# Kernel optimization log

Measured on AMD Instinct MI355X. Metric: run time of the kernel, lower is better.

The kernel has to match this reference:

```python
import jax, jax.numpy as jnp
import numpy as np

D_MODEL = 2048
NUM_EXPERTS = 64
TOP_K = 4
N_TOKENS = 16384


def setup_inputs() -> dict:
    key = jax.random.key(0)
    k_u, k_e = jax.random.split(key)
    u = jax.random.normal(k_u, (N_TOKENS, D_MODEL), dtype=jnp.float32)
    # E initialized like torch.randn(d_model, num_experts) * 0.01
    E = jax.random.normal(k_e, (D_MODEL, NUM_EXPERTS), dtype=jnp.float32) * 0.01
    bias = jnp.zeros((NUM_EXPERTS,), dtype=jnp.float32)
    return {"u": u, "E": E, "bias": bias}


def reference(u, E, bias):
    # logits: [N, num_experts]
    logits = u @ E + bias
    scores = jax.nn.softmax(logits, axis=-1)
    # torch.topk returns values sorted descending; lax.top_k matches
    topk_s, topk_i = jax.lax.top_k(scores, TOP_K)
    aux_loss = jnp.sum(jnp.mean(scores, axis=0) ** 2) * NUM_EXPERTS
    return (topk_i, topk_s, scores, aux_loss)
```

## Files before the change

### kernel.cpp

```cpp
#include <hip/hip_runtime.h>
#include <math.h>

#define N_TOK 16384
#define DM    2048
#define NE    64
#define TOPK  4

#define OFF_TI  0
#define OFF_TS  (N_TOK * TOPK)
#define OFF_SC  (2 * N_TOK * TOPK)
#define OFF_AUX (2 * N_TOK * TOPK + N_TOK * NE)

#define MTPB  16
#define RW    256
#define NRND  (DM / RW)
#define RSTR  264
#define PLN   (MTPB * RSTR)

#define EH_OFF   1024
#define ET_ELEMS ((size_t)NE * DM)
#define WS_NEED  (EH_OFF + 4 * ET_ELEMS)

typedef short s8v __attribute__((ext_vector_type(8)));
typedef float f4v __attribute__((ext_vector_type(4)));

__device__ __forceinline__ unsigned short bf16_rne(float x) {
  unsigned int b = __float_as_uint(x);
  b += 0x7FFFu + ((b >> 16) & 1u);
  return (unsigned short)(b >> 16);
}

__global__ __launch_bounds__(256) void router_prep(
    const float* __restrict__ E, unsigned short* __restrict__ eh,
    unsigned short* __restrict__ el)
{
  __shared__ float t[32][65];
  const int tid = threadIdx.x;
  const int k0  = blockIdx.x * 32;
#pragma unroll
  for (int i = 0; i < 2; ++i) {
    const int fi = i * 256 + tid;
    const int kk = fi >> 4, ee = (fi & 15) * 4;
    const float4 v = *(const float4*)(E + (size_t)(k0 + kk) * NE + ee);
    t[kk][ee] = v.x; t[kk][ee + 1] = v.y; t[kk][ee + 2] = v.z; t[kk][ee + 3] = v.w;
  }
  __syncthreads();
  const int j    = tid >> 6;
  const int lane = tid & 63;
  const int ex   = j * 16 + (lane & 15);
  const int kb   = (lane >> 4) * 8;
  unsigned int hw[4], lw[4];
#pragma unroll
  for (int p = 0; p < 4; ++p) {
    unsigned short h[2], l[2];
#pragma unroll
    for (int q = 0; q < 2; ++q) {
      const float x = t[kb + p * 2 + q][ex];
      h[q] = bf16_rne(x);
      l[q] = bf16_rne(x - __uint_as_float((unsigned)h[q] << 16));
    }
    hw[p] = (unsigned)h[0] | ((unsigned)h[1] << 16);
    lw[p] = (unsigned)l[0] | ((unsigned)l[1] << 16);
  }
  const size_t o = (size_t)blockIdx.x * 2048 + j * 512 + lane * 8;
  *(uint4*)(eh + o) = make_uint4(hw[0], hw[1], hw[2], hw[3]);
  *(uint4*)(el + o) = make_uint4(lw[0], lw[1], lw[2], lw[3]);
}

#define LOAD_U(pf, r) do { _Pragma("unroll") \
  for (int i_ = 0; i_ < 4; ++i_) \
    pf[i_] = *(const float4*)(ugp + (size_t)(r) * RW + i_ * 64); } while (0)

#define WRITE_U(pf, base) do { _Pragma("unroll") \
  for (int i_ = 0; i_ < 4; ++i_) { \
    const float4 v_ = pf[i_]; \
    const unsigned short h0_ = bf16_rne(v_.x), h1_ = bf16_rne(v_.y), \
                         h2_ = bf16_rne(v_.z), h3_ = bf16_rne(v_.w); \
    const unsigned short l0_ = bf16_rne(v_.x - __uint_as_float((unsigned)h0_ << 16)); \
    const unsigned short l1_ = bf16_rne(v_.y - __uint_as_float((unsigned)h1_ << 16)); \
    const unsigned short l2_ = bf16_rne(v_.z - __uint_as_float((unsigned)h2_ << 16)); \
    const unsigned short l3_ = bf16_rne(v_.w - __uint_as_float((unsigned)h3_ << 16)); \
    *(uint2*)&sh[(base) + uoff + i_ * 64] = \
      make_uint2((unsigned)h0_ | ((unsigned)h1_ << 16), (unsigned)h2_ | ((unsigned)h3_ << 16)); \
    *(uint2*)&sh[(base) + PLN + uoff + i_ * 64] = \
      make_uint2((unsigned)l0_ | ((unsigned)l1_ << 16), (unsigned)l2_ | ((unsigned)l3_ << 16)); \
  } } while (0)

#define COMPUTE(r, base) do { _Pragma("unroll") \
  for (int ks_ = 0; ks_ < 2; ++ks_) { \
    const s8v ah_ = *(const s8v*)&sh[(base) + a_off + ks_ * 32]; \
    const s8v al_ = *(const s8v*)&sh[(base) + PLN + a_off + ks_ * 32]; \
    const size_t pb_ = (size_t)(((r) * 8 + kq * 2 + ks_) * 2048) + lane * 8; \
    _Pragma("unroll") for (int j_ = 0; j_ < 4; ++j_) { \
      const s8v bh_ = *(const s8v*)&eh[pb_ + j_ * 512]; \
      const s8v bl_ = *(const s8v*)&el[pb_ + j_ * 512]; \
      acc[j_] = __builtin_amdgcn_mfma_f32_16x16x32_bf16(ah_, bh_, acc[j_], 0, 0, 0); \
      acc[j_] = __builtin_amdgcn_mfma_f32_16x16x32_bf16(ah_, bl_, acc[j_], 0, 0, 0); \
      acc[j_] = __builtin_amdgcn_mfma_f32_16x16x32_bf16(al_, bh_, acc[j_], 0, 0, 0); \
      acc[j_] = __builtin_amdgcn_mfma_f32_16x16x32_bf16(al_, bl_, acc[j_], 0, 0, 0); \
    } } } while (0)

__global__ __launch_bounds__(256, 4) void router_main_mfma(
    const float* __restrict__ u, const unsigned short* __restrict__ eh,
    const unsigned short* __restrict__ el, const float* __restrict__ bias,
    float* __restrict__ out, float* __restrict__ ws)
{
  __shared__ __align__(16) unsigned short sh[4 * PLN];

  const int tid  = threadIdx.x;
  const int lane = tid & 63;
  const int kq   = __builtin_amdgcn_readfirstlane(tid >> 6);
  const int lm   = lane & 15;
  const int lk   = lane >> 4;
  const int tok0 = blockIdx.x * MTPB;

  const int srow = tid >> 4, sseg = tid & 15;
  const float* ugp = u + (size_t)(tok0 + srow) * DM + sseg * 4;
  const int uoff = srow * RSTR + sseg * 4;

  const int a_off = lm * RSTR + kq * 64 + lk * 8;

  f4v acc[4];
#pragma unroll
  for (int j = 0; j < 4; ++j) acc[j] = (f4v){0.f, 0.f, 0.f, 0.f};

  float4 pfA[4], pfB[4];
  LOAD_U(pfA, 0);
  LOAD_U(pfB, 1);
  WRITE_U(pfA, 0);
  __syncthreads();

  for (int rr = 0; rr < NRND; rr += 2) {
    WRITE_U(pfB, 2 * PLN);
    if (rr + 2 < NRND) LOAD_U(pfA, rr + 2);
    COMPUTE(rr, 0);
    __syncthreads();
    if (rr + 2 < NRND) WRITE_U(pfA, 0);
    if (rr + 3 < NRND) LOAD_U(pfB, rr + 3);
    COMPUTE(rr + 1, 2 * PLN);
    __syncthreads();
  }

  float* fin = (float*)sh;
#pragma unroll
  for (int j = 0; j < 4; ++j)
#pragma unroll
    for (int q = 0; q < 4; ++q)
      fin[kq * (16 * 68) + (lk * 4 + q) * 68 + j * 16 + lm] = acc[j][q];
  __syncthreads();

  const float be = bias[lane];
  float asum = 0.f;
#pragma unroll
  for (int tt = 0; tt < 4; ++tt) {
    const int t = kq * 4 + tt;
    float x = fin[t * 68 + lane] + fin[1 * 1088 + t * 68 + lane]
            + fin[2 * 1088 + t * 68 + lane] + fin[3 * 1088 + t * 68 + lane] + be;

    float m = x;
#pragma unroll
    for (int off = 32; off > 0; off >>= 1) m = fmaxf(m, __shfl_xor(m, off));
    float p = expf(x - m);
    float s = p;
#pragma unroll
    for (int off = 32; off > 0; off >>= 1) s += __shfl_xor(s, off);
    float sc = p / s;

    out[OFF_SC + (size_t)(tok0 + t) * NE + lane] = sc;
    asum += sc;

    float v = sc;
#pragma unroll
    for (int k = 0; k < TOPK; ++k) {
      float bv = v;
      int   bi = lane;
#pragma unroll
      for (int off = 32; off > 0; off >>= 1) {
        float ov = __shfl_xor(bv, off);
        int   oi = __shfl_xor(bi, off);
        if (ov > bv || (ov == bv && oi < bi)) { bv = ov; bi = oi; }
      }
      if (lane == k) {
        out[OFF_TI + (size_t)(tok0 + t) * TOPK + k] = (float)bi;
        out[OFF_TS + (size_t)(tok0 + t) * TOPK + k] = bv;
      }
      if (lane == bi) v = -INFINITY;
    }
  }
  atomicAdd(&ws[lane], asum);
}

#define TPB     64
#define FB_DC   32
#define FB_NCH  (1024 / FB_DC)
#define FB_LSTR 68
#define FB_UB   (TPB * FB_LSTR)
#define FB_EOFF (2 * FB_UB)
#define FB_EB   (2 * FB_DC * NE)

__global__ __launch_bounds__(1024, 4) void router_main_fb(
    const float* __restrict__ u, const float* __restrict__ E,
    const float* __restrict__ bias, float* __restrict__ out,
    float* __restrict__ ws)
{
  __shared__ float smem[FB_EOFF + 2 * FB_EB];

  const int tid  = threadIdx.x;
  const int lane = tid & 63;
  const int wid  = __builtin_amdgcn_readfirstlane(tid >> 6);
  const int eg   = wid & 7;
  const int kh   = wid >> 3;
  const int tok0 = blockIdx.x * TPB;

  const int stok  = tid >> 4;
  const int sdseg = tid & 15;
  const int skh   = sdseg >> 3;
  const int sdsub = (sdseg & 7) * 4;
  const float* sgbase = u + (size_t)(tok0 + stok) * DM + skh * 1024 + sdsub;
  float* swp = smem + stok * FB_LSTR + sdseg * 4;

  const int eq  = tid & 511;
  const int ekh = tid >> 9;
  const float* egbase = E + (size_t)ekh * 1024 * NE + eq * 4;
  float* ewp = smem + FB_EOFF + ekh * (FB_DC * NE) + eq * 4;

  float acc[8];
#pragma unroll
  for (int j = 0; j < 8; ++j) acc[j] = 0.f;

  float4 pf[3];
  pf[0] = *(const float4*)(sgbase + 0 * FB_DC);
  pf[1] = *(const float4*)(sgbase + 1 * FB_DC);
  pf[2] = *(const float4*)(sgbase + 2 * FB_DC);
  float4 epf = *(const float4*)(egbase + 0 * (FB_DC * NE));
  *(float4*)(swp + 0) = pf[0];
  *(float4*)(ewp + 0) = epf;
  epf = *(const float4*)(egbase + 1 * (FB_DC * NE));
  __syncthreads();

  for (int c = 0; c < FB_NCH; ++c) {
    if (c + 1 < FB_NCH) {
      *(float4*)(swp + ((c + 1) & 1) * FB_UB) = pf[(c + 1) % 3];
      *(float4*)(ewp + ((c + 1) & 1) * FB_EB) = epf;
    }
    if (c + 2 < FB_NCH)
      epf = *(const float4*)(egbase + (c + 2) * (FB_DC * NE));
    if (c + 3 < FB_NCH)
      pf[c % 3] = *(const float4*)(sgbase + (c + 3) * FB_DC);

    const float* sb = smem + (c & 1) * FB_UB + lane * FB_LSTR + kh * FB_DC;
    const float* eb = smem + FB_EOFF + (c & 1) * FB_EB + kh * (FB_DC * NE) + eg * 8;
#pragma unroll
    for (int s = 0; s < 8; ++s) {
      float4 uf = *(const float4*)(sb + s * 4);
#pragma unroll
      for (int dd = 0; dd < 4; ++dd) {
        const float* er = eb + (s * 4 + dd) * NE;
        float4 e0 = *(const float4*)(er);
        float4 e1 = *(const float4*)(er + 4);
        const float uv = (&uf.x)[dd];
        acc[0] = fmaf(e0.x, uv, acc[0]);
        acc[1] = fmaf(e0.y, uv, acc[1]);
        acc[2] = fmaf(e0.z, uv, acc[2]);
        acc[3] = fmaf(e0.w, uv, acc[3]);
        acc[4] = fmaf(e1.x, uv, acc[4]);
        acc[5] = fmaf(e1.y, uv, acc[5]);
        acc[6] = fmaf(e1.z, uv, acc[6]);
        acc[7] = fmaf(e1.w, uv, acc[7]);
      }
    }
    __syncthreads();
  }

  float* fin = smem;
  if (kh == 0) {
#pragma unroll
    for (int j = 0; j < 8; ++j) fin[lane * 65 + eg * 8 + j] = acc[j];
  }
  __syncthreads();
  if (kh == 1) {
#pragma unroll
    for (int j = 0; j < 8; ++j) fin[lane * 65 + eg * 8 + j] += acc[j];
  }
  __syncthreads();

  const float be = bias[lane];
  float asum = 0.f;
#pragma unroll
  for (int tt = 0; tt < 4; ++tt) {
    const int t = wid * 4 + tt;
    float x = fin[t * 65 + lane] + be;

    float m = x;
#pragma unroll
    for (int off = 32; off > 0; off >>= 1) m = fmaxf(m, __shfl_xor(m, off));
    float p = expf(x - m);
    float s = p;
#pragma unroll
    for (int off = 32; off > 0; off >>= 1) s += __shfl_xor(s, off);
    float sc = p / s;

    out[OFF_SC + (size_t)(tok0 + t) * NE + lane] = sc;
    asum += sc;

    float v = sc;
#pragma unroll
    for (int k = 0; k < TOPK; ++k) {
      float bv = v;
      int   bi = lane;
#pragma unroll
      for (int off = 32; off > 0; off >>= 1) {
        float ov = __shfl_xor(bv, off);
        int   oi = __shfl_xor(bi, off);
        if (ov > bv || (ov == bv && oi < bi)) { bv = ov; bi = oi; }
      }
      if (lane == k) {
        out[OFF_TI + (size_t)(tok0 + t) * TOPK + k] = (float)bi;
        out[OFF_TS + (size_t)(tok0 + t) * TOPK + k] = bv;
      }
      if (lane == bi) v = -INFINITY;
    }
  }
  atomicAdd(&ws[lane], asum);
}

__global__ void router_aux(const float* __restrict__ ws, float* __restrict__ out)
{
  const int lane = threadIdx.x & 63;
  float m = ws[lane] * (1.0f / N_TOK);
  float v = m * m;
#pragma unroll
  for (int off = 32; off > 0; off >>= 1) v += __shfl_xor(v, off);
  if (lane == 0) out[OFF_AUX] = v * (float)NE;
}

extern "C" void kernel_launch(void* const* d_in, const int* in_sizes, int n_in,
                              void* d_out, int out_size, void* d_ws, size_t ws_size,
                              hipStream_t stream) {
  const float* u    = (const float*)d_in[0];
  const float* E    = (const float*)d_in[1];
  const float* bias = (const float*)d_in[2];
  float* out = (float*)d_out;
  float* ws  = (float*)d_ws;

  hipMemsetAsync(ws, 0, NE * sizeof(float), stream);
  if (ws_size >= WS_NEED) {
    unsigned short* eh = (unsigned short*)((char*)ws + EH_OFF);
    unsigned short* el = eh + ET_ELEMS;
    router_prep<<<DM / 32, 256, 0, stream>>>(E, eh, el);
    router_main_mfma<<<N_TOK / MTPB, 256, 0, stream>>>(u, eh, el, bias, out, ws);
  } else {
    router_main_fb<<<N_TOK / TPB, 1024, 0, stream>>>(u, E, bias, out, ws);
  }
  router_aux<<<1, 64, 0, stream>>>(ws, out);
}
```

Before: 313.7 us.

## Enlarge token tile to 64 per block and fuse aux reduction into main kernel

The MFMA router kernel now handles 64 tokens per block instead of 16, using a narrower 128-wide K round. Each wave's E fragments (hi/lo bf16) are reused across four 16-token sub-tiles, so global/L2 traffic for E per token drops fourfold. Cross-wave partial sums are reduced in two passes through shared memory. The workspace memset and the separate aux kernel are replaced by zeroing inside the prep kernel and a last-block-done atomic counter that computes aux_loss. The trade-offs are more accumulator registers (occupancy hint lowered to 1), only 256 blocks in the grid, and a serial 16-token epilogue per wave.

New measurement: 273.6 us. 1.15x faster.

```diff
diff --git a/kernel.cpp b/kernel.cpp
--- a/kernel.cpp
+++ b/kernel.cpp
@@ -11,11 +11,11 @@
 #define OFF_SC  (2 * N_TOK * TOPK)
 #define OFF_AUX (2 * N_TOK * TOPK + N_TOK * NE)
 
-#define MTPB  16
-#define RW    256
+#define MTPB  64
+#define RW    128
 #define NRND  (DM / RW)
-#define RSTR  264
-#define PLN   (MTPB * RSTR)
+#define KSTR  136
+#define PLN   (MTPB * KSTR)
 
 #define EH_OFF   1024
 #define ET_ELEMS ((size_t)NE * DM)
@@ -32,10 +32,11 @@
 
 __global__ __launch_bounds__(256) void router_prep(
     const float* __restrict__ E, unsigned short* __restrict__ eh,
-    unsigned short* __restrict__ el)
+    unsigned short* __restrict__ el, float* __restrict__ ws)
 {
   __shared__ float t[32][65];
   const int tid = threadIdx.x;
+  if (blockIdx.x == 0 && tid < 128) ws[tid] = 0.f;
   const int k0  = blockIdx.x * 32;
 #pragma unroll
   for (int i = 0; i < 2; ++i) {
@@ -68,11 +69,11 @@
 }
 
 #define LOAD_U(pf, r) do { _Pragma("unroll") \
-  for (int i_ = 0; i_ < 4; ++i_) \
-    pf[i_] = *(const float4*)(ugp + (size_t)(r) * RW + i_ * 64); } while (0)
+  for (int i_ = 0; i_ < 8; ++i_) \
+    pf[i_] = *(const float4*)(ugp + (size_t)(r) * RW + i_ * 16); } while (0)
 
 #define WRITE_U(pf, base) do { _Pragma("unroll") \
-  for (int i_ = 0; i_ < 4; ++i_) { \
+  for (int i_ = 0; i_ < 8; ++i_) { \
     const float4 v_ = pf[i_]; \
     const unsigned short h0_ = bf16_rne(v_.x), h1_ = bf16_rne(v_.y), \
                          h2_ = bf16_rne(v_.z), h3_ = bf16_rne(v_.w); \
@@ -80,27 +81,31 @@
     const unsigned short l1_ = bf16_rne(v_.y - __uint_as_float((unsigned)h1_ << 16)); \
     const unsigned short l2_ = bf16_rne(v_.z - __uint_as_float((unsigned)h2_ << 16)); \
     const unsigned short l3_ = bf16_rne(v_.w - __uint_as_float((unsigned)h3_ << 16)); \
-    *(uint2*)&sh[(base) + uoff + i_ * 64] = \
+    *(uint2*)&sh[(base) + uoff + i_ * 16] = \
       make_uint2((unsigned)h0_ | ((unsigned)h1_ << 16), (unsigned)h2_ | ((unsigned)h3_ << 16)); \
-    *(uint2*)&sh[(base) + PLN + uoff + i_ * 64] = \
+    *(uint2*)&sh[(base) + PLN + uoff + i_ * 16] = \
       make_uint2((unsigned)l0_ | ((unsigned)l1_ << 16), (unsigned)l2_ | ((unsigned)l3_ << 16)); \
   } } while (0)
 
-#define COMPUTE(r, base) do { _Pragma("unroll") \
-  for (int ks_ = 0; ks_ < 2; ++ks_) { \
-    const s8v ah_ = *(const s8v*)&sh[(base) + a_off + ks_ * 32]; \
-    const s8v al_ = *(const s8v*)&sh[(base) + PLN + a_off + ks_ * 32]; \
-    const size_t pb_ = (size_t)(((r) * 8 + kq * 2 + ks_) * 2048) + lane * 8; \
+#define COMPUTE(r, base) do { \
+    const int    pk_ = (r) * 4 + kq; \
+    const size_t pb_ = (size_t)pk_ * 2048 + lane * 8; \
+    s8v ah_[4], al_[4]; \
+    _Pragma("unroll") for (int tt_ = 0; tt_ < 4; ++tt_) { \
+      ah_[tt_] = *(const s8v*)&sh[(base) + a_off + tt_ * (16 * KSTR)]; \
+      al_[tt_] = *(const s8v*)&sh[(base) + PLN + a_off + tt_ * (16 * KSTR)]; \
+    } \
     _Pragma("unroll") for (int j_ = 0; j_ < 4; ++j_) { \
       const s8v bh_ = *(const s8v*)&eh[pb_ + j_ * 512]; \
       const s8v bl_ = *(const s8v*)&el[pb_ + j_ * 512]; \
-      acc[j_] = __builtin_amdgcn_mfma_f32_16x16x32_bf16(ah_, bh_, acc[j_], 0, 0, 0); \
-      acc[j_] = __builtin_amdgcn_mfma_f32_16x16x32_bf16(ah_, bl_, acc[j_], 0, 0, 0); \
-      acc[j_] = __builtin_amdgcn_mfma_f32_16x16x32_bf16(al_, bh_, acc[j_], 0, 0, 0); \
-      acc[j_] = __builtin_amdgcn_mfma_f32_16x16x32_bf16(al_, bl_, acc[j_], 0, 0, 0); \
-    } } } while (0)
-
-__global__ __launch_bounds__(256, 4) void router_main_mfma(
+      _Pragma("unroll") for (int tt_ = 0; tt_ < 4; ++tt_) { \
+        acc[tt_][j_] = __builtin_amdgcn_mfma_f32_16x16x32_bf16(ah_[tt_], bh_, acc[tt_][j_], 0, 0, 0); \
+        acc[tt_][j_] = __builtin_amdgcn_mfma_f32_16x16x32_bf16(ah_[tt_], bl_, acc[tt_][j_], 0, 0, 0); \
+        acc[tt_][j_] = __builtin_amdgcn_mfma_f32_16x16x32_bf16(al_[tt_], bh_, acc[tt_][j_], 0, 0, 0); \
+        acc[tt_][j_] = __builtin_amdgcn_mfma_f32_16x16x32_bf16(al_[tt_], bl_, acc[tt_][j_], 0, 0, 0); \
+      } } } while (0)
+
+__global__ __launch_bounds__(256, 1) void router_main_mfma(
     const float* __restrict__ u, const unsigned short* __restrict__ eh,
     const unsigned short* __restrict__ el, const float* __restrict__ bias,
     float* __restrict__ out, float* __restrict__ ws)
@@ -114,17 +119,19 @@
   const int lk   = lane >> 4;
   const int tok0 = blockIdx.x * MTPB;
 
-  const int srow = tid >> 4, sseg = tid & 15;
+  const int srow = tid >> 2, sseg = tid & 3;
   const float* ugp = u + (size_t)(tok0 + srow) * DM + sseg * 4;
-  const int uoff = srow * RSTR + sseg * 4;
-
-  const int a_off = lm * RSTR + kq * 64 + lk * 8;
-
-  f4v acc[4];
-#pragma unroll
-  for (int j = 0; j < 4; ++j) acc[j] = (f4v){0.f, 0.f, 0.f, 0.f};
-
-  float4 pfA[4], pfB[4];
+  const int uoff = srow * KSTR + sseg * 4;
+
+  const int a_off = lm * KSTR + kq * 32 + lk * 8;
+
+  f4v acc[4][4];
+#pragma unroll
+  for (int t = 0; t < 4; ++t)
+#pragma unroll
+    for (int j = 0; j < 4; ++j) acc[t][j] = (f4v){0.f, 0.f, 0.f, 0.f};
+
+  float4 pfA[8], pfB[8];
   LOAD_U(pfA, 0);
   LOAD_U(pfB, 1);
   WRITE_U(pfA, 0);
@@ -142,20 +149,32 @@
   }
 
   float* fin = (float*)sh;
-#pragma unroll
-  for (int j = 0; j < 4; ++j)
-#pragma unroll
-    for (int q = 0; q < 4; ++q)
-      fin[kq * (16 * 68) + (lk * 4 + q) * 68 + j * 16 + lm] = acc[j][q];
+  if (kq < 2) {
+#pragma unroll
+    for (int t = 0; t < 4; ++t)
+#pragma unroll
+      for (int j = 0; j < 4; ++j)
+#pragma unroll
+        for (int q = 0; q < 4; ++q)
+          fin[kq * (64 * 68) + (t * 16 + lk * 4 + q) * 68 + j * 16 + lm] = acc[t][j][q];
+  }
+  __syncthreads();
+  if (kq >= 2) {
+#pragma unroll
+    for (int t = 0; t < 4; ++t)
+#pragma unroll
+      for (int j = 0; j < 4; ++j)
+#pragma unroll
+        for (int q = 0; q < 4; ++q)
+          fin[(kq - 2) * (64 * 68) + (t * 16 + lk * 4 + q) * 68 + j * 16 + lm] += acc[t][j][q];
+  }
   __syncthreads();
 
   const float be = bias[lane];
   float asum = 0.f;
-#pragma unroll
-  for (int tt = 0; tt < 4; ++tt) {
-    const int t = kq * 4 + tt;
-    float x = fin[t * 68 + lane] + fin[1 * 1088 + t * 68 + lane]
-            + fin[2 * 1088 + t * 68 + lane] + fin[3 * 1088 + t * 68 + lane] + be;
+  for (int tt = 0; tt < 16; ++tt) {
+    const int t = kq * 16 + tt;
+    float x = fin[t * 68 + lane] + fin[64 * 68 + t * 68 + lane] + be;
 
     float m = x;
 #pragma unroll
@@ -188,6 +207,22 @@
     }
   }
   atomicAdd(&ws[lane], asum);
+
+  __threadfence();
+  __syncthreads();
+  unsigned* flg = (unsigned*)sh;
+  if (tid == 0) {
+    const unsigned t = atomicAdd((unsigned*)&ws[NE], 1u);
+    flg[9216] = (t == (unsigned)(gridDim.x - 1)) ? 1u : 0u;
+  }
+  __syncthreads();
+  if (flg[9216] && tid < 64) {
+    const float mv = atomicAdd(&ws[tid], 0.f) * (1.0f / N_TOK);
+    float v = mv * mv;
+#pragma unroll
+    for (int off = 32; off > 0; off >>= 1) v += __shfl_xor(v, off);
+    if (tid == 0) out[OFF_AUX] = v * (float)NE;
+  }
 }
 
 #define TPB     64
@@ -343,14 +378,14 @@
   float* out = (float*)d_out;
   float* ws  = (float*)d_ws;
 
-  hipMemsetAsync(ws, 0, NE * sizeof(float), stream);
   if (ws_size >= WS_NEED) {
     unsigned short* eh = (unsigned short*)((char*)ws + EH_OFF);
     unsigned short* el = eh + ET_ELEMS;
-    router_prep<<<DM / 32, 256, 0, stream>>>(E, eh, el);
+    router_prep<<<DM / 32, 256, 0, stream>>>(E, eh, el, ws);
     router_main_mfma<<<N_TOK / MTPB, 256, 0, stream>>>(u, eh, el, bias, out, ws);
   } else {
+    hipMemsetAsync(ws, 0, NE * sizeof(float), stream);
     router_main_fb<<<N_TOK / TPB, 1024, 0, stream>>>(u, E, bias, out, ws);
-  }
-  router_aux<<<1, 64, 0, stream>>>(ws, out);
-}
+    router_aux<<<1, 64, 0, stream>>>(ws, out);
+  }
+}
```
